# Kernel optimization log

Measured on AMD Instinct MI355X. Metric: run time of the kernel, lower is better.

The kernel has to match this reference:

```python
import math
import jax, jax.numpy as jnp
import numpy as np

HIDDEN = 1024
N_HEADS = 16
HEAD = HIDDEN // N_HEADS
B = 2
L = 2048
STRIDE = 128
EXPR = 8
MAXPOS = 2048


def _checkpoint(wi):
    if wi % STRIDE == 0 and wi != 0:
        return wi - EXPR
    return (wi // STRIDE) * STRIDE + STRIDE - EXPR


def _subset_summaries(absolute_max):
    ci = _checkpoint(0)
    s = set()
    while ci <= absolute_max - 1:
        s |= set(range(ci, min(ci + EXPR + 1, absolute_max)))
        ci = _checkpoint(ci + STRIDE)
    return s


def build_sparse_mask(n, bidirectional=True):
    # Faithful numpy port of prepare_sparse_mask: -1e4 everywhere, 0 at allowed positions.
    mask = np.full((n, n), -10000.0, dtype=np.float32)
    global_summaries = _subset_summaries(n) if bidirectional else set()
    for i in range(n):
        absolute_max = n if bidirectional else i + 1
        rounded = ((i + STRIDE) // STRIDE) * STRIDE
        if i % STRIDE == 0 and i != 0:
            s1 = set(range(i - STRIDE, min(absolute_max, i + 1)))
        else:
            s1 = set(range(max(0, rounded - STRIDE), min(absolute_max, rounded + 1)))
        s2 = set() if bidirectional else _subset_summaries(absolute_max)
        idx = sorted(s1 | s2 | global_summaries)
        mask[i, idx] = 0.0
    return mask


def setup_inputs() -> dict:
    key = jax.random.key(0)
    ks = jax.random.split(key, 8)
    s = 1.0 / math.sqrt(HIDDEN)
    inp = {
        "hidden_states": jax.random.normal(ks[0], (B, L, HIDDEN), dtype=jnp.float32),
        "attention_mask": jnp.zeros((B, 1, 1, L), dtype=jnp.float32),
        "Wq": jax.random.normal(ks[1], (HIDDEN, HIDDEN), dtype=jnp.float32) * s,
        "bq": jnp.zeros((HIDDEN,), dtype=jnp.float32),
        "Wk": jax.random.normal(ks[2], (HIDDEN, HIDDEN), dtype=jnp.float32) * s,
        "bk": jnp.zeros((HIDDEN,), dtype=jnp.float32),
        "Wv": jax.random.normal(ks[3], (HIDDEN, HIDDEN), dtype=jnp.float32) * s,
        "bv": jnp.zeros((HIDDEN,), dtype=jnp.float32),
        "sparse_mask": jnp.asarray(build_sparse_mask(MAXPOS)[:L, :L]),
    }
    return inp


def _split_heads(x):  # [B, L, H] -> [B, nH, L, hd]
    b, l, _ = x.shape
    return x.reshape(b, l, N_HEADS, HEAD).transpose(0, 2, 1, 3)


def reference(hidden_states, attention_mask, Wq, bq, Wk, bk, Wv, bv, sparse_mask):
    q = _split_heads(hidden_states @ Wq + bq)
    k = _split_heads(hidden_states @ Wk + bk)
    v = _split_heads(hidden_states @ Wv + bv)
    scores = jnp.einsum("bhqd,bhkd->bhqk", q, k) / math.sqrt(HEAD)
    scores = scores + sparse_mask  # [L,L] broadcasts over [B,nH,L,L]
    scores = jnp.clip(scores, -10000.0, 10000.0)
    scores = scores + attention_mask
    probs = jax.nn.softmax(scores.astype(jnp.float32), axis=-1).astype(scores.dtype)
    # dropout prob = 0.0 -> identity
    ctx = jnp.einsum("bhqk,bhkd->bhqd", probs, v)
    return ctx.transpose(0, 2, 1, 3).reshape(hidden_states.shape[0], -1, HIDDEN)
```

## Files before the change

kernel.cpp:

```cpp
#include <hip/hip_runtime.h>

#define HID 1024
#define NH 16
#define HD 64
#define BB 2
#define LL 2048
#define GC 143
#define GP 192

typedef __attribute__((ext_vector_type(8))) __bf16 bf16x8;
typedef __attribute__((ext_vector_type(4))) float f32x4;

__device__ __forceinline__ void gload_lds16(const void* g, void* l) {
  __builtin_amdgcn_global_load_lds((const __attribute__((address_space(1))) void*)g,
                                   (__attribute__((address_space(3))) void*)l, 16, 0, 0);
}

__global__ __launch_bounds__(256) void cvt_hs_kernel(const float* __restrict__ hs,
                                                     __bf16* __restrict__ hsb) {
  int i = blockIdx.x * 256 + threadIdx.x;
  const float4* src = (const float4*)hs;
  float4 a = src[2 * i], b = src[2 * i + 1];
  bf16x8 v;
  v[0] = (__bf16)a.x; v[1] = (__bf16)a.y; v[2] = (__bf16)a.z; v[3] = (__bf16)a.w;
  v[4] = (__bf16)b.x; v[5] = (__bf16)b.y; v[6] = (__bf16)b.z; v[7] = (__bf16)b.w;
  ((bf16x8*)hsb)[i] = v;
}

__global__ __launch_bounds__(256) void cvt_wt_kernel(const float* __restrict__ Wq,
                                                     const float* __restrict__ Wk,
                                                     const float* __restrict__ Wv,
                                                     __bf16* __restrict__ wtb) {
  int kt = blockIdx.x, nt = blockIdx.y, z = blockIdx.z;
  const float* w = (z == 0) ? Wq : (z == 1) ? Wk : Wv;
  __bf16* dst = wtb + (size_t)z * HID * HID;
  __shared__ __bf16 tile[64][66];
  int t = threadIdx.x;
  int cr = t & 63, rr = t >> 6;
#pragma unroll
  for (int it = 0; it < 16; it++) {
    int r = it * 4 + rr;
    tile[cr][r] = (__bf16)w[(size_t)(kt * 64 + r) * HID + nt * 64 + cr];
  }
  __syncthreads();
#pragma unroll
  for (int it = 0; it < 16; it++) {
    int r = it * 4 + rr;
    dst[(size_t)(nt * 64 + r) * HID + kt * 64 + cr] = tile[r][cr];
  }
}

__global__ __launch_bounds__(256) void setup_kernel(const float* __restrict__ amask,
                                                    unsigned int* __restrict__ zbase,
                                                    float* __restrict__ amg) {
  int i = blockIdx.x * 256 + threadIdx.x;
  zbase[i] = 0u;
  if (i < BB * GP) {
    int b = i / GP, cc = i % GP;
    int k = cc / 9, j = cc - 9 * k;
    int col = (cc < GC) ? (120 + 128 * k + j) : 0;
    amg[i] = amask[b * LL + col];
  }
}

__global__ __launch_bounds__(256, 2) void qkv_gemm_kernel(
    const __bf16* __restrict__ hsb, const __bf16* __restrict__ wtb,
    const float* __restrict__ bq, const float* __restrict__ bk,
    const float* __restrict__ bv, __bf16* __restrict__ qb,
    __bf16* __restrict__ kkb, __bf16* __restrict__ vtb,
    __bf16* __restrict__ kgb, __bf16* __restrict__ vgb) {
  int nt = blockIdx.x, mt = blockIdx.y, which = blockIdx.z;
  const __bf16* wt = wtb + (size_t)which * HID * HID;
  const float* bias = (which == 0) ? bq : (which == 1) ? bk : bv;

  __shared__ __bf16 a_lds[128 * 64];
  __shared__ __bf16 b_lds[128 * 64];

  int tid = threadIdx.x;
  int wave = tid >> 6, lane = tid & 63;
  int wm = wave >> 1, wn = wave & 1;
  int lrow = lane & 15, lgr = lane >> 4, g = lane & 7;

  f32x4 acc[4][4];
#pragma unroll
  for (int i = 0; i < 4; i++)
#pragma unroll
    for (int j = 0; j < 4; j++) acc[i][j] = f32x4{0.f, 0.f, 0.f, 0.f};

  for (int kk = 0; kk < HID; kk += 64) {
#pragma unroll
    for (int i = 0; i < 4; i++) {
      int r = (wave * 4 + i) * 8 + (lane >> 3);
      int gs = (g ^ (r & 7)) * 8;
      gload_lds16(hsb + (size_t)(mt * 128 + r) * HID + kk + gs,
                  &a_lds[(wave * 4 + i) * 512]);
      gload_lds16(wt + (size_t)(nt * 128 + r) * HID + kk + gs,
                  &b_lds[(wave * 4 + i) * 512]);
    }
    __syncthreads();
#pragma unroll
    for (int kf = 0; kf < 2; kf++) {
      bf16x8 af[4], bfr[4];
#pragma unroll
      for (int mr = 0; mr < 4; mr++) {
        int row = wm * 64 + mr * 16 + lrow;
        af[mr] = *(const bf16x8*)((const char*)a_lds + row * 128 +
                                  ((kf * 64 + lgr * 16) ^ ((row & 7) << 4)));
      }
#pragma unroll
      for (int nr = 0; nr < 4; nr++) {
        int row = wn * 64 + nr * 16 + lrow;
        bfr[nr] = *(const bf16x8*)((const char*)b_lds + row * 128 +
                                   ((kf * 64 + lgr * 16) ^ ((row & 7) << 4)));
      }
#pragma unroll
      for (int mr = 0; mr < 4; mr++)
#pragma unroll
        for (int nr = 0; nr < 4; nr++)
          acc[mr][nr] = __builtin_amdgcn_mfma_f32_16x16x32_bf16(
              af[mr], bfr[nr], acc[mr][nr], 0, 0, 0);
    }
    __syncthreads();
  }

#pragma unroll
  for (int nr = 0; nr < 4; nr++) {
    int n = nt * 128 + wn * 64 + nr * 16 + lrow;
    float bsv = bias[n];
    int hh = n >> 6, d = n & 63;
#pragma unroll
    for (int mr = 0; mr < 4; mr++) {
#pragma unroll
      for (int reg = 0; reg < 4; reg++) {
        int m = mt * 128 + wm * 64 + mr * 16 + lgr * 4 + reg;
        int bidx = m >> 11, l = m & 2047;
        float val = acc[mr][nr][reg] + bsv;
        int c7 = l & 127;
        bool isg = (c7 >= 120) || (c7 == 0 && l != 0);
        int cidx = (c7 >= 120) ? ((l >> 7) * 9 + (c7 - 120)) : (((l >> 7) - 1) * 9 + 8);
        if (which == 0) {
          val *= 0.125f;
          qb[((size_t)(bidx * NH + hh) * LL + l) * HD + d] = (__bf16)val;
        } else if (which == 1) {
          __bf16 bv16 = (__bf16)val;
          kkb[((size_t)(bidx * NH + hh) * LL + l) * HD + d] = bv16;
          if (isg) kgb[((size_t)(bidx * NH + hh) * GP + cidx) * HD + d] = bv16;
        } else {
          __bf16 bv16 = (__bf16)val;
          vtb[((size_t)(bidx * NH + hh) * HD + d) * LL + l] = bv16;
          if (isg) vgb[((size_t)(bidx * NH + hh) * HD + d) * GP + cidx] = bv16;
        }
      }
    }
  }
}

__global__ __launch_bounds__(512, 4) void attn_kernel(
    const __bf16* __restrict__ qb, const __bf16* __restrict__ kkb,
    const __bf16* __restrict__ vtb, const __bf16* __restrict__ kgb,
    const __bf16* __restrict__ vgb, const float* __restrict__ amg,
    const float* __restrict__ amask, float* __restrict__ out) {
  __shared__ __bf16 kbuf[2][64 * 64];
  __shared__ __bf16 vbuf[2][64 * 64];
  __shared__ __bf16 p_scr[8][16 * 64];

  int qt = blockIdx.x, hh = blockIdx.y, b = blockIdx.z;
  int tid = threadIdx.x, wave = tid >> 6, lane = tid & 63;
  int lrow = lane & 15, lgr = lane >> 4, g = lane & 7;

  const __bf16* qbh = qb + (size_t)(b * NH + hh) * LL * HD;
  const __bf16* kbh = kkb + (size_t)(b * NH + hh) * LL * HD;
  const __bf16* vth = vtb + (size_t)(b * NH + hh) * HD * LL;
  const __bf16* kgh = kgb + (size_t)(b * NH + hh) * GP * HD;
  const __bf16* vgh = vgb + (size_t)(b * NH + hh) * HD * GP;

  int shift = (qt == 16) ? 0 : 1;
  int qt2 = (qt == 16) ? 0 : qt;
  int W = qt2 * 128;

  int qrow = qt2 * 128 + shift + wave * 16 + lrow;
  int qld = (qrow > LL - 1) ? (LL - 1) : qrow;
  bf16x8 qf0 = *(const bf16x8*)(qbh + (size_t)qld * HD + lgr * 8);
  bf16x8 qf1 = *(const bf16x8*)(qbh + (size_t)qld * HD + 32 + lgr * 8);

  float amG[3][4], amL[2][4];
#pragma unroll
  for (int it = 0; it < 3; it++)
#pragma unroll
    for (int nr = 0; nr < 4; nr++) {
      int cc = it * 64 + nr * 16 + lrow;
      amG[it][nr] = (cc < GC) ? amg[b * GP + cc] : 0.f;
    }
#pragma unroll
  for (int it = 0; it < 2; it++)
#pragma unroll
    for (int nr = 0; nr < 4; nr++)
      amL[it][nr] = amask[b * LL + W + it * 64 + nr * 16 + lrow];

  const float M0 = 20.f;
  float l_part[4];
  f32x4 o_acc[4];
#pragma unroll
  for (int i = 0; i < 4; i++) {
    l_part[i] = 0.f;
    o_acc[i] = f32x4{0.f, 0.f, 0.f, 0.f};
  }
  int myrow = qt2 * 128 + shift + wave * 16 + lgr * 4;

#define STAGE(IT, BI)                                                     \
  do {                                                                    \
    const __bf16 *ks_, *vs_;                                              \
    int vst_;                                                             \
    if ((IT) < 3) {                                                       \
      ks_ = kgh + (size_t)((IT)*64) * HD;                                 \
      vs_ = vgh + (IT)*64;                                                \
      vst_ = GP;                                                          \
    } else {                                                              \
      int cb_ = W + ((IT)-3) * 64;                                        \
      ks_ = kbh + (size_t)cb_ * HD;                                       \
      vs_ = vth + cb_;                                                    \
      vst_ = LL;                                                          \
    }                                                                     \
    int r_ = tid >> 3;                                                    \
    int gs_ = (g ^ (r_ & 7)) * 8;                                         \
    gload_lds16(ks_ + (size_t)r_ * HD + gs_, &kbuf[BI][wave * 512]);      \
    gload_lds16(vs_ + (size_t)r_ * vst_ + gs_, &vbuf[BI][wave * 512]);    \
  } while (0)

  STAGE(0, 0);
  __syncthreads();

#pragma unroll
  for (int it = 0; it < 5; it++) {
    int cur = it & 1;
    if (it < 4) STAGE(it + 1, cur ^ 1);

    const __bf16* k_lds = kbuf[cur];
    const __bf16* v_lds = vbuf[cur];
    int colbase = (it < 3) ? it * 64 : W + (it - 3) * 64;

    f32x4 s[4];
#pragma unroll
    for (int nr = 0; nr < 4; nr++) {
      int row = nr * 16 + lrow;
      bf16x8 kf0 = *(const bf16x8*)((const char*)k_lds + row * 128 +
                                    ((lgr * 16) ^ ((row & 7) << 4)));
      bf16x8 kf1 = *(const bf16x8*)((const char*)k_lds + row * 128 +
                                    ((64 + lgr * 16) ^ ((row & 7) << 4)));
      f32x4 z = f32x4{0.f, 0.f, 0.f, 0.f};
      z = __builtin_amdgcn_mfma_f32_16x16x32_bf16(qf0, kf0, z, 0, 0, 0);
      z = __builtin_amdgcn_mfma_f32_16x16x32_bf16(qf1, kf1, z, 0, 0, 0);
      s[nr] = z;
    }

#pragma unroll
    for (int nr = 0; nr < 4; nr++) {
      if (it < 3) {
        int cc = colbase + nr * 16 + lrow;
        float am = amG[it][nr];
#pragma unroll
        for (int reg = 0; reg < 4; reg++) {
          float v = fminf(fmaxf(s[nr][reg], -10000.f), 10000.f) + am;
          if (cc >= GC) v = -10000.f;
          s[nr][reg] = v;
        }
      } else {
        int off = (it - 3) * 64 + nr * 16 + lrow;
        float am = amL[it - 3][nr];
        bool gcol = (off >= 120) || (off == 0 && W != 0);
#pragma unroll
        for (int reg = 0; reg < 4; reg++) {
          float v = s[nr][reg] + (gcol ? -10000.f : 0.f);
          v = fminf(fmaxf(v, -10000.f), 10000.f) + am;
          s[nr][reg] = v;
        }
      }
    }

#pragma unroll
    for (int reg = 0; reg < 4; reg++) {
#pragma unroll
      for (int nr = 0; nr < 4; nr++) {
        float p = __expf(s[nr][reg] - M0);
        s[nr][reg] = p;
        l_part[reg] += p;
      }
    }

#pragma unroll
    for (int nr = 0; nr < 4; nr++) {
#pragma unroll
      for (int reg = 0; reg < 4; reg++) {
        int rq = lgr * 4 + reg;
        int off = (nr * 32 + lrow * 2) ^ ((rq & 7) << 4);
        *(__bf16*)((char*)&p_scr[wave][0] + rq * 128 + off) = (__bf16)s[nr][reg];
      }
    }
    asm volatile("s_waitcnt lgkmcnt(0)" ::: "memory");
    __builtin_amdgcn_sched_barrier(0);

    bf16x8 pa0 = *(const bf16x8*)((const char*)&p_scr[wave][0] + lrow * 128 +
                                  ((lgr * 16) ^ ((lrow & 7) << 4)));
    bf16x8 pa1 = *(const bf16x8*)((const char*)&p_scr[wave][0] + lrow * 128 +
                                  ((64 + lgr * 16) ^ ((lrow & 7) << 4)));
#pragma unroll
    for (int nd = 0; nd < 4; nd++) {
      int row = nd * 16 + lrow;
      bf16x8 vf0 = *(const bf16x8*)((const char*)v_lds + row * 128 +
                                    ((lgr * 16) ^ ((row & 7) << 4)));
      bf16x8 vf1 = *(const bf16x8*)((const char*)v_lds + row * 128 +
                                    ((64 + lgr * 16) ^ ((row & 7) << 4)));
      o_acc[nd] = __builtin_amdgcn_mfma_f32_16x16x32_bf16(pa0, vf0, o_acc[nd], 0, 0, 0);
      o_acc[nd] = __builtin_amdgcn_mfma_f32_16x16x32_bf16(pa1, vf1, o_acc[nd], 0, 0, 0);
    }
    __syncthreads();
  }
#undef STAGE

#pragma unroll
  for (int off = 1; off < 16; off <<= 1)
#pragma unroll
    for (int reg = 0; reg < 4; reg++) l_part[reg] += __shfl_xor(l_part[reg], off);

#pragma unroll
  for (int nd = 0; nd < 4; nd++) {
#pragma unroll
    for (int reg = 0; reg < 4; reg++) {
      int row = myrow + reg;
      if (row < LL) {
        int d = nd * 16 + lrow;
        out[((size_t)b * LL + row) * HID + hh * HD + d] =
            o_acc[nd][reg] / l_part[reg];
      }
    }
  }
}

extern "C" void kernel_launch(void* const* d_in, const int* in_sizes, int n_in,
                              void* d_out, int out_size, void* d_ws, size_t ws_size,
                              hipStream_t stream) {
  (void)in_sizes; (void)n_in; (void)out_size; (void)ws_size;
  const float* hs = (const float*)d_in[0];
  const float* amask = (const float*)d_in[1];
  const float* Wq = (const float*)d_in[2];
  const float* bq = (const float*)d_in[3];
  const float* Wk = (const float*)d_in[4];
  const float* bk = (const float*)d_in[5];
  const float* Wv = (const float*)d_in[6];
  const float* bv = (const float*)d_in[7];
  float* out = (float*)d_out;

  char* ws = (char*)d_ws;
  __bf16* hsb = (__bf16*)(ws);
  __bf16* wtb = (__bf16*)(ws + 8388608);
  __bf16* qb  = (__bf16*)(ws + 14680064);
  __bf16* kb  = (__bf16*)(ws + 23068672);
  __bf16* vtb = (__bf16*)(ws + 31457280);
  __bf16* kgb = (__bf16*)(ws + 39845888);
  __bf16* vgb = (__bf16*)(ws + 40632320);
  float*  amg = (float*)(ws + 41418752);

  hipLaunchKernelGGL(cvt_hs_kernel, dim3(2048), dim3(256), 0, stream, hs, hsb);
  hipLaunchKernelGGL(cvt_wt_kernel, dim3(16, 16, 3), dim3(256), 0, stream, Wq, Wk, Wv, wtb);
  hipLaunchKernelGGL(setup_kernel, dim3(1536), dim3(256), 0, stream,
                     amask, (unsigned int*)kgb, amg);
  hipLaunchKernelGGL(qkv_gemm_kernel, dim3(8, 32, 3), dim3(256), 0, stream,
                     hsb, wtb, bq, bk, bv, qb, kb, vtb, kgb, vgb);
  hipLaunchKernelGGL(attn_kernel, dim3(17, NH, BB), dim3(512), 0, stream,
                     qb, kb, vtb, kgb, vgb, amg, amask, out);
}
```

Before: 75.23 us.

## Merge prep kernels, precompute mask table, and keep attention probs in registers

```diff
diff --git a/kernel.cpp b/kernel.cpp
--- a/kernel.cpp
+++ b/kernel.cpp
@@ -7,59 +7,76 @@
 #define LL 2048
 #define GC 143
 #define GP 192
+#define AMT_PER_B 2240
 
 typedef __attribute__((ext_vector_type(8))) __bf16 bf16x8;
 typedef __attribute__((ext_vector_type(4))) float f32x4;
+typedef __attribute__((ext_vector_type(4))) int i32x4;
 
 __device__ __forceinline__ void gload_lds16(const void* g, void* l) {
   __builtin_amdgcn_global_load_lds((const __attribute__((address_space(1))) void*)g,
                                    (__attribute__((address_space(3))) void*)l, 16, 0, 0);
 }
 
-__global__ __launch_bounds__(256) void cvt_hs_kernel(const float* __restrict__ hs,
-                                                     __bf16* __restrict__ hsb) {
-  int i = blockIdx.x * 256 + threadIdx.x;
-  const float4* src = (const float4*)hs;
-  float4 a = src[2 * i], b = src[2 * i + 1];
-  bf16x8 v;
-  v[0] = (__bf16)a.x; v[1] = (__bf16)a.y; v[2] = (__bf16)a.z; v[3] = (__bf16)a.w;
-  v[4] = (__bf16)b.x; v[5] = (__bf16)b.y; v[6] = (__bf16)b.z; v[7] = (__bf16)b.w;
-  ((bf16x8*)hsb)[i] = v;
-}
-
-__global__ __launch_bounds__(256) void cvt_wt_kernel(const float* __restrict__ Wq,
-                                                     const float* __restrict__ Wk,
-                                                     const float* __restrict__ Wv,
-                                                     __bf16* __restrict__ wtb) {
-  int kt = blockIdx.x, nt = blockIdx.y, z = blockIdx.z;
-  const float* w = (z == 0) ? Wq : (z == 1) ? Wk : Wv;
-  __bf16* dst = wtb + (size_t)z * HID * HID;
-  __shared__ __bf16 tile[64][66];
+__device__ __forceinline__ unsigned int cvtpk(float lo, float hi) {
+  unsigned int r;
+  asm("v_cvt_pk_bf16_f32 %0, %1, %2" : "=v"(r) : "v"(lo), "v"(hi));
+  return r;
+}
+
+__global__ __launch_bounds__(256) void prep_kernel(
+    const float* __restrict__ hs, __bf16* __restrict__ hsb,
+    const float* __restrict__ Wq, const float* __restrict__ Wk,
+    const float* __restrict__ Wv, __bf16* __restrict__ wtb,
+    const float* __restrict__ amask, unsigned int* __restrict__ zbase,
+    float* __restrict__ amt) {
+  int bx = blockIdx.x;
   int t = threadIdx.x;
-  int cr = t & 63, rr = t >> 6;
-#pragma unroll
-  for (int it = 0; it < 16; it++) {
-    int r = it * 4 + rr;
-    tile[cr][r] = (__bf16)w[(size_t)(kt * 64 + r) * HID + nt * 64 + cr];
-  }
-  __syncthreads();
-#pragma unroll
-  for (int it = 0; it < 16; it++) {
-    int r = it * 4 + rr;
-    dst[(size_t)(nt * 64 + r) * HID + kt * 64 + cr] = tile[r][cr];
-  }
-}
-
-__global__ __launch_bounds__(256) void setup_kernel(const float* __restrict__ amask,
-                                                    unsigned int* __restrict__ zbase,
-                                                    float* __restrict__ amg) {
-  int i = blockIdx.x * 256 + threadIdx.x;
-  zbase[i] = 0u;
-  if (i < BB * GP) {
-    int b = i / GP, cc = i % GP;
-    int k = cc / 9, j = cc - 9 * k;
-    int col = (cc < GC) ? (120 + 128 * k + j) : 0;
-    amg[i] = amask[b * LL + col];
+  if (bx < 2048) {
+    int i = bx * 256 + t;
+    const float4* src = (const float4*)hs;
+    float4 a = src[2 * i], b = src[2 * i + 1];
+    bf16x8 v;
+    v[0] = (__bf16)a.x; v[1] = (__bf16)a.y; v[2] = (__bf16)a.z; v[3] = (__bf16)a.w;
+    v[4] = (__bf16)b.x; v[5] = (__bf16)b.y; v[6] = (__bf16)b.z; v[7] = (__bf16)b.w;
+    ((bf16x8*)hsb)[i] = v;
+  } else if (bx < 2048 + 768) {
+    int z3 = bx - 2048;
+    int kt = z3 & 15, nt = (z3 >> 4) & 15, z = z3 >> 8;
+    const float* w = (z == 0) ? Wq : (z == 1) ? Wk : Wv;
+    __bf16* dst = wtb + (size_t)z * HID * HID;
+    __shared__ __bf16 tile[64][66];
+    int cr = t & 63, rr = t >> 6;
+#pragma unroll
+    for (int it = 0; it < 16; it++) {
+      int r = it * 4 + rr;
+      tile[cr][r] = (__bf16)w[(size_t)(kt * 64 + r) * HID + nt * 64 + cr];
+    }
+    __syncthreads();
+#pragma unroll
+    for (int it = 0; it < 16; it++) {
+      int r = it * 4 + rr;
+      dst[(size_t)(nt * 64 + r) * HID + kt * 64 + cr] = tile[r][cr];
+    }
+  } else if (bx < 2048 + 768 + 1536) {
+    int i = (bx - 2816) * 256 + t;
+    zbase[i] = 0u;
+  } else {
+    int idx = (bx - 4352) * 256 + t;
+    if (idx < BB * AMT_PER_B) {
+      int b = idx / AMT_PER_B, r = idx % AMT_PER_B;
+      float val;
+      if (r < GP) {
+        int k = r / 9, j = r - 9 * k;
+        val = (r < GC) ? (amask[b * LL + 120 + 128 * k + j] - 20.f) : -1e5f;
+      } else {
+        int r2 = r - GP;
+        int w = r2 >> 7, off = r2 & 127;
+        bool gcol = (off >= 120) || (off == 0 && w != 0);
+        val = gcol ? -1e5f : (amask[b * LL + w * 128 + off] - 20.f);
+      }
+      amt[idx] = val;
+    }
   }
 }
 
@@ -155,14 +172,13 @@
   }
 }
 
-__global__ __launch_bounds__(512, 4) void attn_kernel(
+__global__ __launch_bounds__(256, 4) void attn_kernel(
     const __bf16* __restrict__ qb, const __bf16* __restrict__ kkb,
     const __bf16* __restrict__ vtb, const __bf16* __restrict__ kgb,
-    const __bf16* __restrict__ vgb, const float* __restrict__ amg,
-    const float* __restrict__ amask, float* __restrict__ out) {
+    const __bf16* __restrict__ vgb, const float* __restrict__ amt,
+    float* __restrict__ out) {
   __shared__ __bf16 kbuf[2][64 * 64];
   __shared__ __bf16 vbuf[2][64 * 64];
-  __shared__ __bf16 p_scr[8][16 * 64];
 
   int qt = blockIdx.x, hh = blockIdx.y, b = blockIdx.z;
   int tid = threadIdx.x, wave = tid >> 6, lane = tid & 63;
@@ -174,38 +190,25 @@
   const __bf16* kgh = kgb + (size_t)(b * NH + hh) * GP * HD;
   const __bf16* vgh = vgb + (size_t)(b * NH + hh) * HD * GP;
 
-  int shift = (qt == 16) ? 0 : 1;
-  int qt2 = (qt == 16) ? 0 : qt;
-  int W = qt2 * 128;
-
-  int qrow = qt2 * 128 + shift + wave * 16 + lrow;
+  int shift = (qt == 32) ? 0 : 1;
+  int qt2 = (qt == 32) ? 0 : qt;
+  int W = (qt2 >> 1) * 128;
+  const float* amt_b = amt + b * AMT_PER_B;
+  const float* amt_l = amt_b + GP + (qt2 >> 1) * 128;
+
+  int qrow = qt2 * 64 + shift + wave * 16 + lrow;
   int qld = (qrow > LL - 1) ? (LL - 1) : qrow;
   bf16x8 qf0 = *(const bf16x8*)(qbh + (size_t)qld * HD + lgr * 8);
   bf16x8 qf1 = *(const bf16x8*)(qbh + (size_t)qld * HD + 32 + lgr * 8);
 
-  float amG[3][4], amL[2][4];
-#pragma unroll
-  for (int it = 0; it < 3; it++)
-#pragma unroll
-    for (int nr = 0; nr < 4; nr++) {
-      int cc = it * 64 + nr * 16 + lrow;
-      amG[it][nr] = (cc < GC) ? amg[b * GP + cc] : 0.f;
-    }
-#pragma unroll
-  for (int it = 0; it < 2; it++)
-#pragma unroll
-    for (int nr = 0; nr < 4; nr++)
-      amL[it][nr] = amask[b * LL + W + it * 64 + nr * 16 + lrow];
-
-  const float M0 = 20.f;
-  float l_part[4];
+  int va = ((lgr & 1) * 32 + lrow) * 4;
+  int vb = va + 64;
+  bool lohalf = (lane < 32);
+
+  float l_part = 0.f;
   f32x4 o_acc[4];
 #pragma unroll
-  for (int i = 0; i < 4; i++) {
-    l_part[i] = 0.f;
-    o_acc[i] = f32x4{0.f, 0.f, 0.f, 0.f};
-  }
-  int myrow = qt2 * 128 + shift + wave * 16 + lgr * 4;
+  for (int i = 0; i < 4; i++) o_acc[i] = f32x4{0.f, 0.f, 0.f, 0.f};
 
 #define STAGE(IT, BI)                                                     \
   do {                                                                    \
@@ -221,10 +224,13 @@
       vs_ = vth + cb_;                                                    \
       vst_ = LL;                                                          \
     }                                                                     \
-    int r_ = tid >> 3;                                                    \
-    int gs_ = (g ^ (r_ & 7)) * 8;                                         \
-    gload_lds16(ks_ + (size_t)r_ * HD + gs_, &kbuf[BI][wave * 512]);      \
-    gload_lds16(vs_ + (size_t)r_ * vst_ + gs_, &vbuf[BI][wave * 512]);    \
+    _Pragma("unroll")                                                     \
+    for (int i_ = 0; i_ < 2; i_++) {                                      \
+      int r_ = (wave * 2 + i_) * 8 + (lane >> 3);                         \
+      int gs_ = (g ^ (r_ & 7)) * 8;                                       \
+      gload_lds16(ks_ + (size_t)r_ * HD + gs_, &kbuf[BI][(wave * 2 + i_) * 512]); \
+      gload_lds16(vs_ + (size_t)r_ * vst_ + gs_, &vbuf[BI][(wave * 2 + i_) * 512]); \
+    }                                                                     \
   } while (0)
 
   STAGE(0, 0);
@@ -237,7 +243,12 @@
 
     const __bf16* k_lds = kbuf[cur];
     const __bf16* v_lds = vbuf[cur];
-    int colbase = (it < 3) ? it * 64 : W + (it - 3) * 64;
+
+    const float* abase = (it < 3) ? (amt_b + it * 64) : (amt_l + (it - 3) * 64);
+    f32x4 ad[4];
+#pragma unroll
+    for (int nr = 0; nr < 4; nr++)
+      ad[nr] = *(const f32x4*)(abase + nr * 16 + lgr * 4);
 
     f32x4 s[4];
 #pragma unroll
@@ -248,61 +259,58 @@
       bf16x8 kf1 = *(const bf16x8*)((const char*)k_lds + row * 128 +
                                     ((64 + lgr * 16) ^ ((row & 7) << 4)));
       f32x4 z = f32x4{0.f, 0.f, 0.f, 0.f};
-      z = __builtin_amdgcn_mfma_f32_16x16x32_bf16(qf0, kf0, z, 0, 0, 0);
-      z = __builtin_amdgcn_mfma_f32_16x16x32_bf16(qf1, kf1, z, 0, 0, 0);
+      z = __builtin_amdgcn_mfma_f32_16x16x32_bf16(kf0, qf0, z, 0, 0, 0);
+      z = __builtin_amdgcn_mfma_f32_16x16x32_bf16(kf1, qf1, z, 0, 0, 0);
       s[nr] = z;
     }
 
 #pragma unroll
     for (int nr = 0; nr < 4; nr++) {
-      if (it < 3) {
-        int cc = colbase + nr * 16 + lrow;
-        float am = amG[it][nr];
-#pragma unroll
-        for (int reg = 0; reg < 4; reg++) {
-          float v = fminf(fmaxf(s[nr][reg], -10000.f), 10000.f) + am;
-          if (cc >= GC) v = -10000.f;
-          s[nr][reg] = v;
-        }
-      } else {
-        int off = (it - 3) * 64 + nr * 16 + lrow;
-        float am = amL[it - 3][nr];
-        bool gcol = (off >= 120) || (off == 0 && W != 0);
-#pragma unroll
-        for (int reg = 0; reg < 4; reg++) {
-          float v = s[nr][reg] + (gcol ? -10000.f : 0.f);
-          v = fminf(fmaxf(v, -10000.f), 10000.f) + am;
-          s[nr][reg] = v;
-        }
-      }
-    }
-
-#pragma unroll
-    for (int reg = 0; reg < 4; reg++) {
-#pragma unroll
-      for (int nr = 0; nr < 4; nr++) {
-        float p = __expf(s[nr][reg] - M0);
+#pragma unroll
+      for (int reg = 0; reg < 4; reg++) {
+        float v = fminf(fmaxf(s[nr][reg], -10000.f), 10000.f) + ad[nr][reg];
+        float p = __expf(v);
         s[nr][reg] = p;
-        l_part[reg] += p;
-      }
-    }
-
-#pragma unroll
-    for (int nr = 0; nr < 4; nr++) {
-#pragma unroll
-      for (int reg = 0; reg < 4; reg++) {
-        int rq = lgr * 4 + reg;
-        int off = (nr * 32 + lrow * 2) ^ ((rq & 7) << 4);
-        *(__bf16*)((char*)&p_scr[wave][0] + rq * 128 + off) = (__bf16)s[nr][reg];
-      }
-    }
-    asm volatile("s_waitcnt lgkmcnt(0)" ::: "memory");
-    __builtin_amdgcn_sched_barrier(0);
-
-    bf16x8 pa0 = *(const bf16x8*)((const char*)&p_scr[wave][0] + lrow * 128 +
-                                  ((lgr * 16) ^ ((lrow & 7) << 4)));
-    bf16x8 pa1 = *(const bf16x8*)((const char*)&p_scr[wave][0] + lrow * 128 +
-                                  ((64 + lgr * 16) ^ ((lrow & 7) << 4)));
+        l_part += p;
+      }
+    }
+
+    unsigned int c00 = cvtpk(s[0][0], s[0][1]), c01 = cvtpk(s[0][2], s[0][3]);
+    unsigned int c10 = cvtpk(s[1][0], s[1][1]), c11 = cvtpk(s[1][2], s[1][3]);
+    unsigned int c20 = cvtpk(s[2][0], s[2][1]), c21 = cvtpk(s[2][2], s[2][3]);
+    unsigned int c30 = cvtpk(s[3][0], s[3][1]), c31 = cvtpk(s[3][2], s[3][3]);
+
+    i32x4 w0, w1;
+    {
+      int a0 = __builtin_amdgcn_ds_bpermute(va, (int)c00);
+      int a1 = __builtin_amdgcn_ds_bpermute(va, (int)c10);
+      w0[0] = lohalf ? a0 : a1;
+      int b0 = __builtin_amdgcn_ds_bpermute(va, (int)c01);
+      int b1 = __builtin_amdgcn_ds_bpermute(va, (int)c11);
+      w0[1] = lohalf ? b0 : b1;
+      int d0 = __builtin_amdgcn_ds_bpermute(vb, (int)c00);
+      int d1 = __builtin_amdgcn_ds_bpermute(vb, (int)c10);
+      w0[2] = lohalf ? d0 : d1;
+      int e0 = __builtin_amdgcn_ds_bpermute(vb, (int)c01);
+      int e1 = __builtin_amdgcn_ds_bpermute(vb, (int)c11);
+      w0[3] = lohalf ? e0 : e1;
+
+      int f0 = __builtin_amdgcn_ds_bpermute(va, (int)c20);
+      int f1 = __builtin_amdgcn_ds_bpermute(va, (int)c30);
+      w1[0] = lohalf ? f0 : f1;
+      int g0 = __builtin_amdgcn_ds_bpermute(va, (int)c21);
+      int g1 = __builtin_amdgcn_ds_bpermute(va, (int)c31);
+      w1[1] = lohalf ? g0 : g1;
+      int h0 = __builtin_amdgcn_ds_bpermute(vb, (int)c20);
+      int h1 = __builtin_amdgcn_ds_bpermute(vb, (int)c30);
+      w1[2] = lohalf ? h0 : h1;
+      int i0 = __builtin_amdgcn_ds_bpermute(vb, (int)c21);
+      int i1 = __builtin_amdgcn_ds_bpermute(vb, (int)c31);
+      w1[3] = lohalf ? i0 : i1;
+    }
+    bf16x8 pb0 = __builtin_bit_cast(bf16x8, w0);
+    bf16x8 pb1 = __builtin_bit_cast(bf16x8, w1);
+
 #pragma unroll
     for (int nd = 0; nd < 4; nd++) {
       int row = nd * 16 + lrow;
@@ -310,28 +318,27 @@
                                     ((lgr * 16) ^ ((row & 7) << 4)));
       bf16x8 vf1 = *(const bf16x8*)((const char*)v_lds + row * 128 +
                                     ((64 + lgr * 16) ^ ((row & 7) << 4)));
-      o_acc[nd] = __builtin_amdgcn_mfma_f32_16x16x32_bf16(pa0, vf0, o_acc[nd], 0, 0, 0);
-      o_acc[nd] = __builtin_amdgcn_mfma_f32_16x16x32_bf16(pa1, vf1, o_acc[nd], 0, 0, 0);
+      o_acc[nd] = __builtin_amdgcn_mfma_f32_16x16x32_bf16(vf0, pb0, o_acc[nd], 0, 0, 0);
+      o_acc[nd] = __builtin_amdgcn_mfma_f32_16x16x32_bf16(vf1, pb1, o_acc[nd], 0, 0, 0);
     }
     __syncthreads();
   }
 #undef STAGE
 
-#pragma unroll
-  for (int off = 1; off < 16; off <<= 1)
-#pragma unroll
-    for (int reg = 0; reg < 4; reg++) l_part[reg] += __shfl_xor(l_part[reg], off);
-
-#pragma unroll
-  for (int nd = 0; nd < 4; nd++) {
-#pragma unroll
-    for (int reg = 0; reg < 4; reg++) {
-      int row = myrow + reg;
-      if (row < LL) {
-        int d = nd * 16 + lrow;
-        out[((size_t)b * LL + row) * HID + hh * HD + d] =
-            o_acc[nd][reg] / l_part[reg];
-      }
+  l_part += __shfl_xor(l_part, 16);
+  l_part += __shfl_xor(l_part, 32);
+  float rl = 1.f / l_part;
+
+  if (qrow < LL) {
+    float* obase = out + ((size_t)b * LL + qrow) * HID + hh * HD + lgr * 4;
+#pragma unroll
+    for (int nd = 0; nd < 4; nd++) {
+      float4 ov;
+      ov.x = o_acc[nd][0] * rl;
+      ov.y = o_acc[nd][1] * rl;
+      ov.z = o_acc[nd][2] * rl;
+      ov.w = o_acc[nd][3] * rl;
+      *(float4*)(obase + nd * 16) = ov;
     }
   }
 }
@@ -358,14 +365,12 @@
   __bf16* vtb = (__bf16*)(ws + 31457280);
   __bf16* kgb = (__bf16*)(ws + 39845888);
   __bf16* vgb = (__bf16*)(ws + 40632320);
-  float*  amg = (float*)(ws + 41418752);
-
-  hipLaunchKernelGGL(cvt_hs_kernel, dim3(2048), dim3(256), 0, stream, hs, hsb);
-  hipLaunchKernelGGL(cvt_wt_kernel, dim3(16, 16, 3), dim3(256), 0, stream, Wq, Wk, Wv, wtb);
-  hipLaunchKernelGGL(setup_kernel, dim3(1536), dim3(256), 0, stream,
-                     amask, (unsigned int*)kgb, amg);
+  float*  amt = (float*)(ws + 41418752);
+
+  hipLaunchKernelGGL(prep_kernel, dim3(4370), dim3(256), 0, stream,
+                     hs, hsb, Wq, Wk, Wv, wtb, amask, (unsigned int*)kgb, amt);
   hipLaunchKernelGGL(qkv_gemm_kernel, dim3(8, 32, 3), dim3(256), 0, stream,
                      hsb, wtb, bq, bk, bv, qb, kb, vtb, kgb, vgb);
-  hipLaunchKernelGGL(attn_kernel, dim3(17, NH, BB), dim3(512), 0, stream,
-                     qb, kb, vtb, kgb, vgb, amg, amask, out);
-}
+  hipLaunchKernelGGL(attn_kernel, dim3(33, NH, BB), dim3(256), 0, stream,
+                     qb, kb, vtb, kgb, vgb, amt, out);
+}
```

Result: faster. 70.59 us (-6.2%).
